# Optimization experiments

Measured on AMD Instinct MI355X. Metric: run time of the kernel, lower is better.

Reference implementation:

```python
import jax, jax.numpy as jnp
import numpy as np

N_NODES = 100000
FEAT_DIM = 256
MAX_DEG = 128
BATCH = 512          # per side (batch1, batch2)
S1 = 10              # layer-2 fanout (1-hop samples)
S2 = 25              # layer-1 fanout (2-hop samples)
HID = 256            # per-branch output dim; concat -> 512


def setup_inputs() -> dict:
    key = jax.random.key(0)
    ks = jax.random.split(key, 10)
    return {
        "features": jax.random.normal(ks[0], (N_NODES, FEAT_DIM), jnp.float32),
        "Ws1": jax.random.normal(ks[1], (FEAT_DIM, HID), jnp.float32) * 0.05,
        "Wn1": jax.random.normal(ks[2], (FEAT_DIM, HID), jnp.float32) * 0.05,
        "Ws2": jax.random.normal(ks[3], (2 * HID, HID), jnp.float32) * 0.05,
        "Wn2": jax.random.normal(ks[4], (2 * HID, HID), jnp.float32) * 0.05,
        "adj": jax.random.randint(ks[5], (N_NODES, MAX_DEG), 0, N_NODES, jnp.int32),
        "batch1": jax.random.randint(ks[6], (BATCH,), 0, N_NODES, jnp.int32),
        "batch2": jax.random.randint(ks[7], (BATCH,), 0, N_NODES, jnp.int32),
        "col1": jax.random.randint(ks[8], (2 * BATCH, S1), 0, MAX_DEG, jnp.int32),
        "col2": jax.random.randint(ks[9], (2 * BATCH * S1, S2), 0, MAX_DEG, jnp.int32),
    }


def _l2_normalize(x, eps=1e-12):
    return x * jax.lax.rsqrt(jnp.maximum(jnp.sum(x * x, axis=1, keepdims=True), eps))


def _mean_agg(h_self, h_neigh, fanout, Ws, Wn, act):
    # h_self: [M, d_in]; h_neigh: [M*fanout, d_in]
    neigh_mean = h_neigh.reshape(h_self.shape[0], fanout, -1).mean(axis=1)
    return act(jnp.concatenate([h_self @ Ws, neigh_mean @ Wn], axis=1))


def reference(features, Ws1, Wn1, Ws2, Wn2, adj, batch1, batch2, col1, col2):
    nodes = jnp.concatenate([batch1, batch2])                  # [2B]
    # uniform neighbor sampling via gather into preprocessed adjacency table
    s1 = jnp.take_along_axis(adj[nodes], col1, axis=1).reshape(-1)   # [2B*S1]
    s2 = jnp.take_along_axis(adj[s1], col2, axis=1).reshape(-1)      # [2B*S1*S2]
    h0 = features[nodes]      # [2B, D]
    h1 = features[s1]         # [2B*S1, D]
    h2 = features[s2]         # [2B*S1*S2, D]
    # GraphSAGE layer 1 (relu, concat)
    h0_new = _mean_agg(h0, h1, S1, Ws1, Wn1, jax.nn.relu)      # [2B, 2H]
    h1_new = _mean_agg(h1, h2, S2, Ws1, Wn1, jax.nn.relu)      # [2B*S1, 2H]
    # GraphSAGE layer 2 (identity act, concat)
    out = _mean_agg(h0_new, h1_new, S1, Ws2, Wn2, lambda x: x)  # [2B, 2H]
    out = _l2_normalize(out)
    return out  # rows [:BATCH] = outputs1, rows [BATCH:] = outputs2
```

## Files before the change

kernel.cpp:

```cpp
#include <hip/hip_runtime.h>
#include <hip/hip_bf16.h>

#define NB2    1024
#define FS1    10
#define FS2    25
#define FD     256
#define FH     256
#define MAXDEG 128

typedef __attribute__((ext_vector_type(8))) short bf16x8;
typedef __attribute__((ext_vector_type(4))) float f32x4;

__device__ inline ushort f2bf(float f) {
    union { float f; unsigned u; } v; v.f = f;
    unsigned u = v.u;
    unsigned r = (u + 0x7FFFu + ((u >> 16) & 1u)) >> 16;
    return (ushort)r;
}
__device__ inline float bf2f(ushort h) {
    union { unsigned u; float f; } v; v.u = ((unsigned)h) << 16;
    return v.f;
}

__global__ void prep_kernel(const float* __restrict__ Ws1, const float* __restrict__ Wn1,
                            const float* __restrict__ Ws2, const float* __restrict__ Wn2,
                            ushort* __restrict__ Wt_s1, ushort* __restrict__ Wt_n1,
                            ushort* __restrict__ Wt_s2, ushort* __restrict__ Wt_n2,
                            const int* __restrict__ batch1, const int* __restrict__ batch2,
                            const int* __restrict__ adj,
                            const int* __restrict__ col1, const int* __restrict__ col2,
                            int* __restrict__ nodes, int* __restrict__ s1,
                            int* __restrict__ s2)
{
    int b = blockIdx.x;
    if (b < 1536) {
        int t = b * 256 + threadIdx.x;
        const float* W; ushort* Wt; int K; int base;
        if (t < 131072) {
            K = 256;
            if (t < 65536) { W = Ws1; Wt = Wt_s1; base = 0; }
            else           { W = Wn1; Wt = Wt_n1; base = 65536; }
        } else {
            K = 512;
            if (t < 262144) { W = Ws2; Wt = Wt_s2; base = 131072; }
            else            { W = Wn2; Wt = Wt_n2; base = 262144; }
        }
        int tt = t - base;
        int k = tt >> 8;
        int n = tt & 255;
        Wt[(long)n * K + k] = f2bf(W[tt]);
    } else {
        int t2 = (b - 1536) * 256 + threadIdx.x;
        int i  = t2 / FS2;
        int ns = i / FS1;
        int node = (ns < 512) ? batch1[ns] : batch2[ns - 512];
        int s1v = adj[(long)node * MAXDEG + col1[i]];
        s2[t2] = adj[(long)s1v * MAXDEG + col2[t2]];
        if (t2 - i * FS2 == 0) {
            s1[i] = s1v;
            if (i - ns * FS1 == 0) nodes[ns] = node;
        }
    }
}

template<int F>
__device__ __forceinline__ void mean_body(const float* __restrict__ src,
                                          const int* __restrict__ idx,
                                          ushort* __restrict__ dst,
                                          int g, int l)
{
    const int* ip = idx + (long)g * F;
    int r[F];
    #pragma unroll
    for (int j = 0; j < F; ++j) r[j] = ip[j];

    float4 acc[4];
    #pragma unroll
    for (int q = 0; q < 4; ++q) acc[q] = make_float4(0.f, 0.f, 0.f, 0.f);

    #pragma unroll
    for (int j0 = 0; j0 < F; j0 += 8) {
        float4 v[8];
        #pragma unroll
        for (int u = 0; u < 8; ++u)
            if (j0 + u < F)
                v[u] = *((const float4*)(src + (long)r[j0 + u] * FD) + l);
        #pragma unroll
        for (int u = 0; u < 8; ++u)
            if (j0 + u < F) {
                int q = u & 3;
                acc[q].x += v[u].x; acc[q].y += v[u].y;
                acc[q].z += v[u].z; acc[q].w += v[u].w;
            }
    }
    float s = 1.0f / F;
    float sx = (acc[0].x + acc[1].x + acc[2].x + acc[3].x) * s;
    float sy = (acc[0].y + acc[1].y + acc[2].y + acc[3].y) * s;
    float sz = (acc[0].z + acc[1].z + acc[2].z + acc[3].z) * s;
    float sw = (acc[0].w + acc[1].w + acc[2].w + acc[3].w) * s;
    uint2 o;
    o.x = (unsigned)f2bf(sx) | ((unsigned)f2bf(sy) << 16);
    o.y = (unsigned)f2bf(sz) | ((unsigned)f2bf(sw) << 16);
    *((uint2*)(dst + (long)g * FD) + l) = o;
}

__global__ void means_kernel(const float* __restrict__ features,
                             const int* __restrict__ s2, const int* __restrict__ s1,
                             ushort* __restrict__ nm2, ushort* __restrict__ nm1)
{
    int wb = blockIdx.x;
    int wave = threadIdx.x >> 6;
    int l = threadIdx.x & 63;
    if (wb < 2560) mean_body<FS2>(features, s2, nm2, wb * 4 + wave, l);
    else           mean_body<FS1>(features, s1, nm1, (wb - 2560) * 4 + wave, l);
}

__global__ void l1gemm_kernel(const float* __restrict__ features,
                              const ushort* __restrict__ nm2, const ushort* __restrict__ nm1,
                              const int* __restrict__ s1, const int* __restrict__ nodes,
                              const ushort* __restrict__ Wt_s1, const ushort* __restrict__ Wt_n1,
                              ushort* __restrict__ h1n, ushort* __restrict__ h0n)
{
    const int wave = threadIdx.x >> 6;
    const int l    = threadIdx.x & 63;
    const int m16  = l & 15;
    const int g    = l >> 4;
    int u = blockIdx.x * 4 + wave;
    const int cs = u & 3;
    int t = u >> 2;

    int self;
    const ushort* An = nullptr;
    const int* idx = nullptr;
    const ushort* Bt;
    ushort* C;
    int coff;
    if (t < 640)       { self = 1; idx = s1;    C = h1n; Bt = Wt_s1; coff = 0; }
    else if (t < 1280) { self = 0; t -= 640;  An = nm2; C = h1n; Bt = Wt_n1; coff = 256; }
    else if (t < 1344) { self = 1; t -= 1280; idx = nodes; C = h0n; Bt = Wt_s1; coff = 0; }
    else               { self = 0; t -= 1344; An = nm1; C = h0n; Bt = Wt_n1; coff = 256; }

    const int r0  = t * 16;
    const int row = r0 + m16;
    const long arow = self ? (long)idx[row] : (long)row;

    f32x4 acc[4];
    #pragma unroll
    for (int j = 0; j < 4; ++j) acc[j] = (f32x4){0.f, 0.f, 0.f, 0.f};

    #pragma unroll
    for (int k0 = 0; k0 < 256; k0 += 32) {
        bf16x8 a;
        if (self) {
            const float* p = features + arow * FD + k0 + g * 8;
            float4 v0 = *(const float4*)p;
            float4 v1 = *(const float4*)(p + 4);
            a[0] = (short)f2bf(v0.x); a[1] = (short)f2bf(v0.y);
            a[2] = (short)f2bf(v0.z); a[3] = (short)f2bf(v0.w);
            a[4] = (short)f2bf(v1.x); a[5] = (short)f2bf(v1.y);
            a[6] = (short)f2bf(v1.z); a[7] = (short)f2bf(v1.w);
        } else {
            a = *(const bf16x8*)(An + arow * FD + k0 + g * 8);
        }
        #pragma unroll
        for (int j = 0; j < 4; ++j) {
            bf16x8 bf = *(const bf16x8*)(Bt + (long)(cs * 64 + j * 16 + m16) * 256 + k0 + g * 8);
            acc[j] = __builtin_amdgcn_mfma_f32_16x16x32_bf16(a, bf, acc[j], 0, 0, 0);
        }
    }

    #pragma unroll
    for (int j = 0; j < 4; ++j) {
        #pragma unroll
        for (int r = 0; r < 4; ++r) {
            int rr = r0 + g * 4 + r;
            int cc = coff + cs * 64 + j * 16 + m16;
            C[(long)rr * 512 + cc] = f2bf(fmaxf(acc[j][r], 0.f));
        }
    }
}

__global__ void mean_bf16_kernel(const ushort* __restrict__ src,
                                 ushort* __restrict__ dst,
                                 int F, int G)
{
    int g = blockIdx.x * 4 + (threadIdx.x >> 6);
    if (g >= G) return;
    int l = threadIdx.x & 63;
    float acc[8] = {};
    for (int j = 0; j < F; ++j) {
        uint4 v = *((const uint4*)(src + ((long)g * F + j) * 512) + l);
        unsigned w[4] = { v.x, v.y, v.z, v.w };
        #pragma unroll
        for (int q = 0; q < 4; ++q) {
            acc[2 * q]     += bf2f((ushort)(w[q] & 0xFFFF));
            acc[2 * q + 1] += bf2f((ushort)(w[q] >> 16));
        }
    }
    float s = 1.0f / F;
    uint4 o;
    unsigned* ow = (unsigned*)&o;
    #pragma unroll
    for (int q = 0; q < 4; ++q)
        ow[q] = (unsigned)f2bf(acc[2 * q] * s) | ((unsigned)f2bf(acc[2 * q + 1] * s) << 16);
    *((uint4*)(dst + (long)g * 512) + l) = o;
}

__global__ void l2gemm_kernel(const ushort* __restrict__ h0n, const ushort* __restrict__ ml2,
                              const ushort* __restrict__ Wt_s2, const ushort* __restrict__ Wt_n2,
                              float* __restrict__ opre)
{
    const int wave = threadIdx.x >> 6;
    const int l    = threadIdx.x & 63;
    const int m16  = l & 15;
    const int g    = l >> 4;
    int u = blockIdx.x * 4 + wave;
    const int kh  = u & 3;
    const int cs  = (u >> 2) & 3;
    const int rt  = (u >> 4) & 63;
    const int sub = u >> 10;

    const ushort* A  = sub ? ml2 : h0n;
    const ushort* Bt = sub ? Wt_n2 : Wt_s2;
    const int coff   = sub ? 256 : 0;

    const int r0  = rt * 16;
    const int row = r0 + m16;
    const int kb  = kh * 128;

    f32x4 acc[4];
    #pragma unroll
    for (int j = 0; j < 4; ++j) acc[j] = (f32x4){0.f, 0.f, 0.f, 0.f};

    #pragma unroll
    for (int ks = 0; ks < 128; ks += 32) {
        int k = kb + ks;
        bf16x8 a = *(const bf16x8*)(A + (long)row * 512 + k + g * 8);
        #pragma unroll
        for (int j = 0; j < 4; ++j) {
            bf16x8 bf = *(const bf16x8*)(Bt + (long)(cs * 64 + j * 16 + m16) * 512 + k + g * 8);
            acc[j] = __builtin_amdgcn_mfma_f32_16x16x32_bf16(a, bf, acc[j], 0, 0, 0);
        }
    }

    float* op = opre + (long)kh * NB2 * 512;
    #pragma unroll
    for (int j = 0; j < 4; ++j) {
        #pragma unroll
        for (int r = 0; r < 4; ++r) {
            int rr = r0 + g * 4 + r;
            int cc = coff + cs * 64 + j * 16 + m16;
            op[(long)rr * 512 + cc] = acc[j][r];
        }
    }
}

__global__ void l2norm_kernel(const float* __restrict__ in, float* __restrict__ out)
{
    int r = blockIdx.x;
    int t = threadIdx.x;
    long i0 = (long)r * 512 + t;
    const long P = (long)NB2 * 512;
    float v0 = in[i0]       + in[i0 + P]       + in[i0 + 2*P]       + in[i0 + 3*P];
    float v1 = in[i0 + 256] + in[i0 + P + 256] + in[i0 + 2*P + 256] + in[i0 + 3*P + 256];
    float s = v0 * v0 + v1 * v1;
    #pragma unroll
    for (int o = 32; o > 0; o >>= 1) s += __shfl_down(s, o, 64);
    __shared__ float wsum[4];
    if ((t & 63) == 0) wsum[t >> 6] = s;
    __syncthreads();
    float tot = wsum[0] + wsum[1] + wsum[2] + wsum[3];
    float inv = rsqrtf(fmaxf(tot, 1e-12f));
    out[r * 512 + t] = v0 * inv;
    out[r * 512 + 256 + t] = v1 * inv;
}

extern "C" void kernel_launch(void* const* d_in, const int* in_sizes, int n_in,
                              void* d_out, int out_size, void* d_ws, size_t ws_size,
                              hipStream_t stream)
{
    const float* features = (const float*)d_in[0];
    const float* Ws1      = (const float*)d_in[1];
    const float* Wn1      = (const float*)d_in[2];
    const float* Ws2      = (const float*)d_in[3];
    const float* Wn2      = (const float*)d_in[4];
    const int*   adj      = (const int*)d_in[5];
    const int*   batch1   = (const int*)d_in[6];
    const int*   batch2   = (const int*)d_in[7];
    const int*   col1     = (const int*)d_in[8];
    const int*   col2     = (const int*)d_in[9];
    float* out = (float*)d_out;

    char* w = (char*)d_ws;
    auto alloc = [&](size_t bytes) {
        char* p = w;
        w += (bytes + 255) & ~(size_t)255;
        return p;
    };
    int*    nodes = (int*)alloc((size_t)NB2 * 4);
    int*    s1    = (int*)alloc((size_t)NB2 * FS1 * 4);
    int*    s2    = (int*)alloc((size_t)NB2 * FS1 * FS2 * 4);
    ushort* nm1   = (ushort*)alloc((size_t)NB2 * FD * 2);
    ushort* nm2   = (ushort*)alloc((size_t)NB2 * FS1 * FD * 2);
    ushort* h0n   = (ushort*)alloc((size_t)NB2 * 512 * 2);
    ushort* h1n   = (ushort*)alloc((size_t)NB2 * FS1 * 512 * 2);
    ushort* ml2   = (ushort*)alloc((size_t)NB2 * 512 * 2);
    float*  opre  = (float*)alloc((size_t)4 * NB2 * 512 * 4);
    ushort* Wt_s1 = (ushort*)alloc((size_t)FD * FH * 2);
    ushort* Wt_n1 = (ushort*)alloc((size_t)FD * FH * 2);
    ushort* Wt_s2 = (ushort*)alloc((size_t)512 * FH * 2);
    ushort* Wt_n2 = (ushort*)alloc((size_t)512 * FH * 2);

    prep_kernel<<<2536, 256, 0, stream>>>(Ws1, Wn1, Ws2, Wn2,
                                          Wt_s1, Wt_n1, Wt_s2, Wt_n2,
                                          batch1, batch2, adj, col1, col2,
                                          nodes, s1, s2);

    means_kernel<<<2816, 256, 0, stream>>>(features, s2, s1, nm2, nm1);

    l1gemm_kernel<<<1408, 256, 0, stream>>>(features, nm2, nm1, s1, nodes,
                                            Wt_s1, Wt_n1, h1n, h0n);

    mean_bf16_kernel<<<NB2 / 4, 256, 0, stream>>>(h1n, ml2, FS1, NB2);

    l2gemm_kernel<<<512, 256, 0, stream>>>(h0n, ml2, Wt_s2, Wt_n2, opre);

    l2norm_kernel<<<NB2, 256, 0, stream>>>(opre, out);
}
```

Measured before the change: 98.26 us.

## Regroup kernel stages so independent self-GEMMs run alongside mean reductions

```diff
diff --git a/kernel.cpp b/kernel.cpp
--- a/kernel.cpp
+++ b/kernel.cpp
@@ -104,45 +104,15 @@
     *((uint2*)(dst + (long)g * FD) + l) = o;
 }
 
-__global__ void means_kernel(const float* __restrict__ features,
-                             const int* __restrict__ s2, const int* __restrict__ s1,
-                             ushort* __restrict__ nm2, ushort* __restrict__ nm1)
-{
-    int wb = blockIdx.x;
-    int wave = threadIdx.x >> 6;
-    int l = threadIdx.x & 63;
-    if (wb < 2560) mean_body<FS2>(features, s2, nm2, wb * 4 + wave, l);
-    else           mean_body<FS1>(features, s1, nm1, (wb - 2560) * 4 + wave, l);
-}
-
-__global__ void l1gemm_kernel(const float* __restrict__ features,
-                              const ushort* __restrict__ nm2, const ushort* __restrict__ nm1,
-                              const int* __restrict__ s1, const int* __restrict__ nodes,
-                              const ushort* __restrict__ Wt_s1, const ushort* __restrict__ Wt_n1,
-                              ushort* __restrict__ h1n, ushort* __restrict__ h0n)
-{
-    const int wave = threadIdx.x >> 6;
-    const int l    = threadIdx.x & 63;
-    const int m16  = l & 15;
-    const int g    = l >> 4;
-    int u = blockIdx.x * 4 + wave;
-    const int cs = u & 3;
-    int t = u >> 2;
-
-    int self;
-    const ushort* An = nullptr;
-    const int* idx = nullptr;
-    const ushort* Bt;
-    ushort* C;
-    int coff;
-    if (t < 640)       { self = 1; idx = s1;    C = h1n; Bt = Wt_s1; coff = 0; }
-    else if (t < 1280) { self = 0; t -= 640;  An = nm2; C = h1n; Bt = Wt_n1; coff = 256; }
-    else if (t < 1344) { self = 1; t -= 1280; idx = nodes; C = h0n; Bt = Wt_s1; coff = 0; }
-    else               { self = 0; t -= 1344; An = nm1; C = h0n; Bt = Wt_n1; coff = 256; }
-
-    const int r0  = t * 16;
+__device__ __forceinline__ void l1gemm_self_wave(const float* __restrict__ features,
+                                                 const int* __restrict__ idx,
+                                                 const ushort* __restrict__ Bt,
+                                                 ushort* __restrict__ C,
+                                                 int r0, int cs, int coff,
+                                                 int m16, int g)
+{
     const int row = r0 + m16;
-    const long arow = self ? (long)idx[row] : (long)row;
+    const long arow = (long)idx[row];
 
     f32x4 acc[4];
     #pragma unroll
@@ -150,84 +120,64 @@
 
     #pragma unroll
     for (int k0 = 0; k0 < 256; k0 += 32) {
+        const float* p = features + arow * FD + k0 + g * 8;
+        float4 v0 = *(const float4*)p;
+        float4 v1 = *(const float4*)(p + 4);
         bf16x8 a;
-        if (self) {
-            const float* p = features + arow * FD + k0 + g * 8;
-            float4 v0 = *(const float4*)p;
-            float4 v1 = *(const float4*)(p + 4);
-            a[0] = (short)f2bf(v0.x); a[1] = (short)f2bf(v0.y);
-            a[2] = (short)f2bf(v0.z); a[3] = (short)f2bf(v0.w);
-            a[4] = (short)f2bf(v1.x); a[5] = (short)f2bf(v1.y);
-            a[6] = (short)f2bf(v1.z); a[7] = (short)f2bf(v1.w);
-        } else {
-            a = *(const bf16x8*)(An + arow * FD + k0 + g * 8);
-        }
+        a[0] = (short)f2bf(v0.x); a[1] = (short)f2bf(v0.y);
+        a[2] = (short)f2bf(v0.z); a[3] = (short)f2bf(v0.w);
+        a[4] = (short)f2bf(v1.x); a[5] = (short)f2bf(v1.y);
+        a[6] = (short)f2bf(v1.z); a[7] = (short)f2bf(v1.w);
         #pragma unroll
         for (int j = 0; j < 4; ++j) {
             bf16x8 bf = *(const bf16x8*)(Bt + (long)(cs * 64 + j * 16 + m16) * 256 + k0 + g * 8);
             acc[j] = __builtin_amdgcn_mfma_f32_16x16x32_bf16(a, bf, acc[j], 0, 0, 0);
         }
     }
-
-    #pragma unroll
-    for (int j = 0; j < 4; ++j) {
-        #pragma unroll
-        for (int r = 0; r < 4; ++r) {
-            int rr = r0 + g * 4 + r;
-            int cc = coff + cs * 64 + j * 16 + m16;
-            C[(long)rr * 512 + cc] = f2bf(fmaxf(acc[j][r], 0.f));
-        }
-    }
-}
-
-__global__ void mean_bf16_kernel(const ushort* __restrict__ src,
-                                 ushort* __restrict__ dst,
-                                 int F, int G)
-{
-    int g = blockIdx.x * 4 + (threadIdx.x >> 6);
-    if (g >= G) return;
-    int l = threadIdx.x & 63;
-    float acc[8] = {};
-    for (int j = 0; j < F; ++j) {
-        uint4 v = *((const uint4*)(src + ((long)g * F + j) * 512) + l);
-        unsigned w[4] = { v.x, v.y, v.z, v.w };
-        #pragma unroll
-        for (int q = 0; q < 4; ++q) {
-            acc[2 * q]     += bf2f((ushort)(w[q] & 0xFFFF));
-            acc[2 * q + 1] += bf2f((ushort)(w[q] >> 16));
-        }
-    }
-    float s = 1.0f / F;
-    uint4 o;
-    unsigned* ow = (unsigned*)&o;
-    #pragma unroll
-    for (int q = 0; q < 4; ++q)
-        ow[q] = (unsigned)f2bf(acc[2 * q] * s) | ((unsigned)f2bf(acc[2 * q + 1] * s) << 16);
-    *((uint4*)(dst + (long)g * 512) + l) = o;
-}
-
-__global__ void l2gemm_kernel(const ushort* __restrict__ h0n, const ushort* __restrict__ ml2,
-                              const ushort* __restrict__ Wt_s2, const ushort* __restrict__ Wt_n2,
-                              float* __restrict__ opre)
-{
-    const int wave = threadIdx.x >> 6;
-    const int l    = threadIdx.x & 63;
-    const int m16  = l & 15;
-    const int g    = l >> 4;
-    int u = blockIdx.x * 4 + wave;
-    const int kh  = u & 3;
-    const int cs  = (u >> 2) & 3;
-    const int rt  = (u >> 4) & 63;
-    const int sub = u >> 10;
-
-    const ushort* A  = sub ? ml2 : h0n;
-    const ushort* Bt = sub ? Wt_n2 : Wt_s2;
-    const int coff   = sub ? 256 : 0;
-
-    const int r0  = rt * 16;
+    #pragma unroll
+    for (int j = 0; j < 4; ++j)
+        #pragma unroll
+        for (int r = 0; r < 4; ++r)
+            C[(long)(r0 + g * 4 + r) * 512 + coff + cs * 64 + j * 16 + m16] =
+                f2bf(fmaxf(acc[j][r], 0.f));
+}
+
+__device__ __forceinline__ void l1gemm_neigh_wave(const ushort* __restrict__ An,
+                                                  const ushort* __restrict__ Bt,
+                                                  ushort* __restrict__ C,
+                                                  int r0, int cs, int coff,
+                                                  int m16, int g)
+{
+    const int row = r0 + m16;
+    f32x4 acc[4];
+    #pragma unroll
+    for (int j = 0; j < 4; ++j) acc[j] = (f32x4){0.f, 0.f, 0.f, 0.f};
+
+    #pragma unroll
+    for (int k0 = 0; k0 < 256; k0 += 32) {
+        bf16x8 a = *(const bf16x8*)(An + (long)row * FD + k0 + g * 8);
+        #pragma unroll
+        for (int j = 0; j < 4; ++j) {
+            bf16x8 bf = *(const bf16x8*)(Bt + (long)(cs * 64 + j * 16 + m16) * 256 + k0 + g * 8);
+            acc[j] = __builtin_amdgcn_mfma_f32_16x16x32_bf16(a, bf, acc[j], 0, 0, 0);
+        }
+    }
+    #pragma unroll
+    for (int j = 0; j < 4; ++j)
+        #pragma unroll
+        for (int r = 0; r < 4; ++r)
+            C[(long)(r0 + g * 4 + r) * 512 + coff + cs * 64 + j * 16 + m16] =
+                f2bf(fmaxf(acc[j][r], 0.f));
+}
+
+__device__ __forceinline__ void l2gemm_wave(const ushort* __restrict__ A,
+                                            const ushort* __restrict__ Bt,
+                                            float* __restrict__ op,
+                                            int r0, int cs, int kh, int coff,
+                                            int m16, int g)
+{
     const int row = r0 + m16;
     const int kb  = kh * 128;
-
     f32x4 acc[4];
     #pragma unroll
     for (int j = 0; j < 4; ++j) acc[j] = (f32x4){0.f, 0.f, 0.f, 0.f};
@@ -242,17 +192,90 @@
             acc[j] = __builtin_amdgcn_mfma_f32_16x16x32_bf16(a, bf, acc[j], 0, 0, 0);
         }
     }
-
-    float* op = opre + (long)kh * NB2 * 512;
-    #pragma unroll
-    for (int j = 0; j < 4; ++j) {
-        #pragma unroll
-        for (int r = 0; r < 4; ++r) {
-            int rr = r0 + g * 4 + r;
-            int cc = coff + cs * 64 + j * 16 + m16;
-            op[(long)rr * 512 + cc] = acc[j][r];
-        }
-    }
+    #pragma unroll
+    for (int j = 0; j < 4; ++j)
+        #pragma unroll
+        for (int r = 0; r < 4; ++r)
+            op[(long)(r0 + g * 4 + r) * 512 + coff + cs * 64 + j * 16 + m16] = acc[j][r];
+}
+
+__global__ void k2_means_l1self(const float* __restrict__ features,
+                                const int* __restrict__ s2, const int* __restrict__ s1,
+                                const int* __restrict__ nodes,
+                                ushort* __restrict__ nm2, ushort* __restrict__ nm1,
+                                const ushort* __restrict__ Wt_s1,
+                                ushort* __restrict__ h1n, ushort* __restrict__ h0n)
+{
+    int b = blockIdx.x;
+    int wave = threadIdx.x >> 6;
+    int l = threadIdx.x & 63;
+    if (b < 2560) { mean_body<FS2>(features, s2, nm2, b * 4 + wave, l); return; }
+    if (b < 2816) { mean_body<FS1>(features, s1, nm1, (b - 2816 + 256) * 4 + wave, l); return; }
+    int u = (b - 2816) * 4 + wave;
+    int cs = u & 3;
+    int t = u >> 2;
+    int m16 = l & 15, g = l >> 4;
+    if (t < 640) l1gemm_self_wave(features, s1,    Wt_s1, h1n, t * 16,        cs, 0, m16, g);
+    else         l1gemm_self_wave(features, nodes, Wt_s1, h0n, (t - 640) * 16, cs, 0, m16, g);
+}
+
+__global__ void k3_l1neigh(const ushort* __restrict__ nm2, const ushort* __restrict__ nm1,
+                           const ushort* __restrict__ Wt_n1,
+                           ushort* __restrict__ h1n, ushort* __restrict__ h0n)
+{
+    int u = blockIdx.x * 4 + (threadIdx.x >> 6);
+    int l = threadIdx.x & 63;
+    int cs = u & 3;
+    int t = u >> 2;
+    int m16 = l & 15, g = l >> 4;
+    if (t < 640) l1gemm_neigh_wave(nm2, Wt_n1, h1n, t * 16,        cs, 256, m16, g);
+    else         l1gemm_neigh_wave(nm1, Wt_n1, h0n, (t - 640) * 16, cs, 256, m16, g);
+}
+
+__global__ void k4_ml2_l2self(const ushort* __restrict__ h1n, ushort* __restrict__ ml2,
+                              const ushort* __restrict__ h0n,
+                              const ushort* __restrict__ Wt_s2,
+                              float* __restrict__ opre)
+{
+    int b = blockIdx.x;
+    int wave = threadIdx.x >> 6;
+    int l = threadIdx.x & 63;
+    if (b < 256) {
+        int gp = b * 4 + wave;
+        float acc[8] = {};
+        for (int j = 0; j < FS1; ++j) {
+            uint4 v = *((const uint4*)(h1n + ((long)gp * FS1 + j) * 512) + l);
+            unsigned wd[4] = { v.x, v.y, v.z, v.w };
+            #pragma unroll
+            for (int q = 0; q < 4; ++q) {
+                acc[2 * q]     += bf2f((ushort)(wd[q] & 0xFFFF));
+                acc[2 * q + 1] += bf2f((ushort)(wd[q] >> 16));
+            }
+        }
+        float s = 1.0f / FS1;
+        uint4 o;
+        unsigned* ow = (unsigned*)&o;
+        #pragma unroll
+        for (int q = 0; q < 4; ++q)
+            ow[q] = (unsigned)f2bf(acc[2 * q] * s) | ((unsigned)f2bf(acc[2 * q + 1] * s) << 16);
+        *((uint4*)(ml2 + (long)gp * 512) + l) = o;
+        return;
+    }
+    int u = (b - 256) * 4 + wave;
+    int kh = u & 3, cs = (u >> 2) & 3, rt = u >> 4;
+    int m16 = l & 15, g = l >> 4;
+    l2gemm_wave(h0n, Wt_s2, opre + (long)kh * NB2 * 512, rt * 16, cs, kh, 0, m16, g);
+}
+
+__global__ void k5_l2neigh(const ushort* __restrict__ ml2,
+                           const ushort* __restrict__ Wt_n2,
+                           float* __restrict__ opre)
+{
+    int u = blockIdx.x * 4 + (threadIdx.x >> 6);
+    int l = threadIdx.x & 63;
+    int kh = u & 3, cs = (u >> 2) & 3, rt = u >> 4;
+    int m16 = l & 15, g = l >> 4;
+    l2gemm_wave(ml2, Wt_n2, opre + (long)kh * NB2 * 512, rt * 16, cs, kh, 256, m16, g);
 }
 
 __global__ void l2norm_kernel(const float* __restrict__ in, float* __restrict__ out)
@@ -316,14 +339,14 @@
                                           batch1, batch2, adj, col1, col2,
                                           nodes, s1, s2);
 
-    means_kernel<<<2816, 256, 0, stream>>>(features, s2, s1, nm2, nm1);
-
-    l1gemm_kernel<<<1408, 256, 0, stream>>>(features, nm2, nm1, s1, nodes,
-                                            Wt_s1, Wt_n1, h1n, h0n);
-
-    mean_bf16_kernel<<<NB2 / 4, 256, 0, stream>>>(h1n, ml2, FS1, NB2);
-
-    l2gemm_kernel<<<512, 256, 0, stream>>>(h0n, ml2, Wt_s2, Wt_n2, opre);
+    k2_means_l1self<<<3520, 256, 0, stream>>>(features, s2, s1, nodes,
+                                              nm2, nm1, Wt_s1, h1n, h0n);
+
+    k3_l1neigh<<<704, 256, 0, stream>>>(nm2, nm1, Wt_n1, h1n, h0n);
+
+    k4_ml2_l2self<<<512, 256, 0, stream>>>(h1n, ml2, h0n, Wt_s2, opre);
+
+    k5_l2neigh<<<256, 256, 0, stream>>>(ml2, Wt_n2, opre);
 
     l2norm_kernel<<<NB2, 256, 0, stream>>>(opre, out);
 }
```

After: 98.68 us. About the same (+0.4%).
